# Optimization experiments

Measured on AMD Instinct MI355X. Metric: run time of the kernel, lower is better.

## Reference

```python
import jax, jax.numpy as jnp
import numpy as np

B, L, D = 2048, 64, 300   # batch, words per sentence, embedding dim (== kernel_size)
C = 512                    # conv out_channels
H, O = 2048, 1             # fc hidden, fc output


def setup_inputs() -> dict:
    key = jax.random.key(0)
    ks = jax.random.split(key, 8)
    s = 0.05
    return {
        "x1": jax.random.normal(ks[0], (B, L, D), jnp.float32),
        "x2": jax.random.normal(ks[1], (B, L, D), jnp.float32),
        # Conv1d(in=1, out=C, kernel=D) weight is [C,1,D]; stored as [C,D]
        "Wc": jax.random.normal(ks[2], (C, D), jnp.float32) * s,
        "bc": jax.random.normal(ks[3], (C,), jnp.float32) * s,
        "W1": jax.random.normal(ks[4], (H, 2 * C), jnp.float32) * s,
        "b1": jax.random.normal(ks[5], (H,), jnp.float32) * s,
        "W2": jax.random.normal(ks[6], (O, H), jnp.float32) * s,
        "b2": jax.random.normal(ks[7], (O,), jnp.float32) * s,
    }


def reference(x1, x2, Wc, bc, W1, b1, W2, b2):
    # Per-word Conv1d(kernel=D) + ReLU is a full-width filter == linear map D->C.
    # Batch all words in one einsum instead of the original Python loop.
    def encode(x):
        h = jax.nn.relu(jnp.einsum('bld,cd->blc', x, Wc) + bc)  # [B,L,C]
        return jnp.max(h, axis=1)                                # max over words -> [B,C]

    e1 = encode(x1)
    e2 = encode(x2)
    feat = jnp.concatenate([e1 - e2, e1 * e2], axis=1)           # [B,2C]
    h = jnp.tanh(feat @ W1.T + b1)                               # [B,H]
    return h @ W2.T + b2                                         # [B,O]
```

## Files before the change

kernel.cpp:

```cpp
#include <hip/hip_runtime.h>


#define B_SZ 2048
#define L_SZ 64
#define D_SZ 300
#define C_SZ 512
#define H_SZ 2048
#define KPAD 320
#define NKC 40
#define LDSPITCH 328

typedef __bf16 bf16x8 __attribute__((ext_vector_type(8)));
typedef float f32x4 __attribute__((ext_vector_type(4)));

__device__ __forceinline__ unsigned short f2bf(float f) {
  unsigned int u = __float_as_uint(f);
  u += 0x7fffu + ((u >> 16) & 1u);
  return (unsigned short)(u >> 16);
}

__global__ __launch_bounds__(256)
void convert_kernel(const float* __restrict__ Wc, const float* __restrict__ W1,
                    unsigned short* __restrict__ WcSwz, unsigned short* __restrict__ W1Swz) {
  int id = blockIdx.x * 256 + threadIdx.x;
  if (id < C_SZ * NKC) {
    int c = id / NKC, kc = id - c * NKC;
    unsigned short tmp[8];
    #pragma unroll
    for (int i = 0; i < 8; ++i) {
      int k = kc * 8 + i;
      tmp[i] = (k < D_SZ) ? f2bf(Wc[c * D_SZ + k]) : (unsigned short)0;
    }
    unsigned short* dst = WcSwz + (((c >> 4) * NKC + kc) * 16 + (c & 15)) * 8;
    *reinterpret_cast<uint4*>(dst) = *reinterpret_cast<uint4*>(tmp);
    return;
  }
  id -= C_SZ * NKC;
  if (id < H_SZ * 128) {
    int j = id >> 7, kc = id & 127;
    const float* src = W1 + (size_t)j * 1024 + kc * 8;
    unsigned short tmp[8];
    #pragma unroll
    for (int i = 0; i < 8; ++i) tmp[i] = f2bf(src[i]);
    unsigned short* dst = W1Swz + (((j >> 4) * 128 + kc) * 16 + (j & 15)) * 8;
    *reinterpret_cast<uint4*>(dst) = *reinterpret_cast<uint4*>(tmp);
  }
}

__global__ __launch_bounds__(256)
void encode_kernel(const float* __restrict__ x1, const float* __restrict__ x2,
                   const unsigned short* __restrict__ WcSwz,
                   const float* __restrict__ bc, float* __restrict__ e) {
  const int b = blockIdx.x, z = blockIdx.y;
  const float* __restrict__ x = (z ? x2 : x1) + (size_t)b * (L_SZ * D_SZ);
  __shared__ unsigned short xs[L_SZ * LDSPITCH];
  const int tid = threadIdx.x;

  const float4* __restrict__ xv = reinterpret_cast<const float4*>(x);
  for (int i = tid; i < (L_SZ * D_SZ / 4); i += 256) {
    float4 v = xv[i];
    int word = i / 75, col = (i - word * 75) * 4;
    unsigned int lo = (unsigned int)f2bf(v.x) | ((unsigned int)f2bf(v.y) << 16);
    unsigned int hi = (unsigned int)f2bf(v.z) | ((unsigned int)f2bf(v.w) << 16);
    *reinterpret_cast<uint2*>(&xs[word * LDSPITCH + col]) = make_uint2(lo, hi);
  }
  for (int i = tid; i < L_SZ * (KPAD - D_SZ); i += 256) {
    int word = i / 20, c = D_SZ + (i - word * 20);
    xs[word * LDSPITCH + c] = 0;
  }
  __syncthreads();

  const int wave = tid >> 6, lane = tid & 63;
  const int l16 = lane & 15, quad = lane >> 4;
  const int koff = quad * 8;

  f32x4 acc[4][8];
  #pragma unroll
  for (int mt = 0; mt < 4; ++mt)
    #pragma unroll
    for (int nt = 0; nt < 8; ++nt)
      #pragma unroll
      for (int r = 0; r < 4; ++r) acc[mt][nt][r] = 0.f;

  #pragma unroll
  for (int ks = 0; ks < KPAD / 32; ++ks) {
    bf16x8 a[4];
    #pragma unroll
    for (int mt = 0; mt < 4; ++mt)
      a[mt] = *reinterpret_cast<const bf16x8*>(&xs[(mt * 16 + l16) * LDSPITCH + ks * 32 + koff]);
    #pragma unroll
    for (int nt = 0; nt < 8; ++nt) {
      const unsigned short* bp =
          WcSwz + ((((wave * 8 + nt) * NKC) + ks * 4 + quad) * 16 + l16) * 8;
      bf16x8 bw = *reinterpret_cast<const bf16x8*>(bp);
      #pragma unroll
      for (int mt = 0; mt < 4; ++mt)
        acc[mt][nt] = __builtin_amdgcn_mfma_f32_16x16x32_bf16(a[mt], bw, acc[mt][nt], 0, 0, 0);
    }
  }

  #pragma unroll
  for (int nt = 0; nt < 8; ++nt) {
    int c = wave * 128 + nt * 16 + l16;
    float bias = bc[c];
    float v = 0.f;
    #pragma unroll
    for (int mt = 0; mt < 4; ++mt)
      #pragma unroll
      for (int r = 0; r < 4; ++r)
        v = fmaxf(v, acc[mt][nt][r] + bias);
    v = fmaxf(v, __shfl_xor(v, 16));
    v = fmaxf(v, __shfl_xor(v, 32));
    if (quad == 0)
      e[((size_t)z * B_SZ + b) * C_SZ + c] = v;
  }
}

__global__ __launch_bounds__(256)
void feat_kernel(const float* __restrict__ e, unsigned short* __restrict__ featSwz) {
  int id = blockIdx.x * 256 + threadIdx.x;
  if (id >= B_SZ * 128) return;
  int b = id >> 7, kc = id & 127;
  unsigned short tmp[8];
  #pragma unroll
  for (int i = 0; i < 8; ++i) {
    int k = kc * 8 + i, c = k & 511;
    float a = e[(size_t)b * C_SZ + c];
    float bb = e[(size_t)B_SZ * C_SZ + (size_t)b * C_SZ + c];
    tmp[i] = f2bf((k < C_SZ) ? (a - bb) : (a * bb));
  }
  unsigned short* dst = featSwz + (((b >> 4) * 128 + kc) * 16 + (b & 15)) * 8;
  *reinterpret_cast<uint4*>(dst) = *reinterpret_cast<uint4*>(tmp);
}

__global__ __launch_bounds__(256, 4)
void fc1_kernel(const unsigned short* __restrict__ featSwz,
                const unsigned short* __restrict__ W1Swz,
                const float* __restrict__ b1, const float* __restrict__ W2,
                float* __restrict__ partial) {
  const int mbase = blockIdx.x * 32;
  const int tid = threadIdx.x;
  const int wave = tid >> 6, lane = tid & 63;
  const int l16 = lane & 15, quad = lane >> 4;
  const int nbase = blockIdx.y * 128 + wave * 32;

  f32x4 acc[2][2];
  #pragma unroll
  for (int mt = 0; mt < 2; ++mt)
    #pragma unroll
    for (int nt = 0; nt < 2; ++nt)
      #pragma unroll
      for (int r = 0; r < 4; ++r) acc[mt][nt][r] = 0.f;

  #pragma unroll 4
  for (int ks = 0; ks < 32; ++ks) {
    bf16x8 a[2], bw[2];
    #pragma unroll
    for (int mt = 0; mt < 2; ++mt)
      a[mt] = *reinterpret_cast<const bf16x8*>(
          featSwz + (((size_t)(blockIdx.x * 2 + mt) * 128 + ks * 4 + quad) * 16 + l16) * 8);
    #pragma unroll
    for (int nt = 0; nt < 2; ++nt)
      bw[nt] = *reinterpret_cast<const bf16x8*>(
          W1Swz + (((size_t)(blockIdx.y * 8 + wave * 2 + nt) * 128 + ks * 4 + quad) * 16 + l16) * 8);
    #pragma unroll
    for (int mt = 0; mt < 2; ++mt)
      #pragma unroll
      for (int nt = 0; nt < 2; ++nt)
        acc[mt][nt] = __builtin_amdgcn_mfma_f32_16x16x32_bf16(a[mt], bw[nt], acc[mt][nt], 0, 0, 0);
  }

  float c[2][4];
  #pragma unroll
  for (int mt = 0; mt < 2; ++mt)
    #pragma unroll
    for (int r = 0; r < 4; ++r) c[mt][r] = 0.f;

  #pragma unroll
  for (int nt = 0; nt < 2; ++nt) {
    int j = nbase + nt * 16 + l16;
    float bias = b1[j];
    float w2 = W2[j];
    #pragma unroll
    for (int mt = 0; mt < 2; ++mt)
      #pragma unroll
      for (int r = 0; r < 4; ++r) {
        float pre = acc[mt][nt][r] + bias;
        pre = fminf(fmaxf(pre, -15.f), 15.f);
        float ex = __expf(2.f * pre);
        c[mt][r] += w2 * ((ex - 1.f) / (ex + 1.f));
      }
  }
  #pragma unroll
  for (int off = 1; off <= 8; off <<= 1)
    #pragma unroll
    for (int mt = 0; mt < 2; ++mt)
      #pragma unroll
      for (int r = 0; r < 4; ++r)
        c[mt][r] += __shfl_xor(c[mt][r], off);

  if (l16 == 0) {
    int slice = blockIdx.y * 4 + wave;
    #pragma unroll
    for (int mt = 0; mt < 2; ++mt)
      #pragma unroll
      for (int r = 0; r < 4; ++r) {
        int brow = mbase + mt * 16 + quad * 4 + r;
        partial[(size_t)slice * B_SZ + brow] = c[mt][r];
      }
  }
}

__global__ __launch_bounds__(256)
void finalize_kernel(const float* __restrict__ partial, const float* __restrict__ b2,
                     float* __restrict__ out) {
  int b = blockIdx.x * 256 + threadIdx.x;
  float s = b2[0];
  #pragma unroll 8
  for (int i = 0; i < 64; ++i) s += partial[(size_t)i * B_SZ + b];
  out[b] = s;
}

extern "C" void kernel_launch(void* const* d_in, const int* in_sizes, int n_in,
                              void* d_out, int out_size, void* d_ws, size_t ws_size,
                              hipStream_t stream) {
  const float* x1 = (const float*)d_in[0];
  const float* x2 = (const float*)d_in[1];
  const float* Wc = (const float*)d_in[2];
  const float* bc = (const float*)d_in[3];
  const float* W1 = (const float*)d_in[4];
  const float* b1 = (const float*)d_in[5];
  const float* W2 = (const float*)d_in[6];
  const float* b2 = (const float*)d_in[7];

  char* ws = (char*)d_ws;
  unsigned short* WcSwz   = (unsigned short*)(ws);
  unsigned short* W1Swz   = (unsigned short*)(ws + 327680);
  float*          e       = (float*)(ws + 4521984);
  unsigned short* featSwz = (unsigned short*)(ws + 12910592);
  float*          partial = (float*)(ws + 17104896);

  {
    int total = C_SZ * NKC + H_SZ * 128;
    convert_kernel<<<(total + 255) / 256, 256, 0, stream>>>(Wc, W1, WcSwz, W1Swz);
  }
  encode_kernel<<<dim3(B_SZ, 2), 256, 0, stream>>>(x1, x2, WcSwz, bc, e);
  feat_kernel<<<(B_SZ * 128 + 255) / 256, 256, 0, stream>>>(e, featSwz);
  fc1_kernel<<<dim3(B_SZ / 32, H_SZ / 128), 256, 0, stream>>>(featSwz, W1Swz, b1, W2, partial);
  finalize_kernel<<<B_SZ / 256, 256, 0, stream>>>(partial, b2, (float*)d_out);
}
```

Baseline: 489.3 us.

## K-major swizzled layouts, register double-buffering, and larger fc1 tiles

Reorders the swizzled bf16 layouts of Wc, W1 and feat so that the k-chunk index is outermost, giving contiguous loads per k-step. Both the encode and fc1 MFMA loops now prefetch the next k-step's operands into registers while the current step computes. fc1 tiles grow from 32x32 to 64x64 per wave-group, halving the number of partial slices that finalize has to reduce. Register pressure rises, so launch bounds are set to 2 blocks per CU, which lowers occupancy.

```diff
diff --git a/kernel.cpp b/kernel.cpp
--- a/kernel.cpp
+++ b/kernel.cpp
@@ -31,7 +31,7 @@
       int k = kc * 8 + i;
       tmp[i] = (k < D_SZ) ? f2bf(Wc[c * D_SZ + k]) : (unsigned short)0;
     }
-    unsigned short* dst = WcSwz + (((c >> 4) * NKC + kc) * 16 + (c & 15)) * 8;
+    unsigned short* dst = WcSwz + (((kc * 32 + (c >> 4)) * 16) + (c & 15)) * 8;
     *reinterpret_cast<uint4*>(dst) = *reinterpret_cast<uint4*>(tmp);
     return;
   }
@@ -42,12 +42,12 @@
     unsigned short tmp[8];
     #pragma unroll
     for (int i = 0; i < 8; ++i) tmp[i] = f2bf(src[i]);
-    unsigned short* dst = W1Swz + (((j >> 4) * 128 + kc) * 16 + (j & 15)) * 8;
+    unsigned short* dst = W1Swz + (((kc * 128 + (j >> 4)) * 16) + (j & 15)) * 8;
     *reinterpret_cast<uint4*>(dst) = *reinterpret_cast<uint4*>(tmp);
   }
 }
 
-__global__ __launch_bounds__(256)
+__global__ __launch_bounds__(256, 2)
 void encode_kernel(const float* __restrict__ x1, const float* __restrict__ x2,
                    const unsigned short* __restrict__ WcSwz,
                    const float* __restrict__ bc, float* __restrict__ e) {
@@ -72,7 +72,6 @@
 
   const int wave = tid >> 6, lane = tid & 63;
   const int l16 = lane & 15, quad = lane >> 4;
-  const int koff = quad * 8;
 
   f32x4 acc[4][8];
   #pragma unroll
@@ -82,20 +81,37 @@
       #pragma unroll
       for (int r = 0; r < 4; ++r) acc[mt][nt][r] = 0.f;
 
+  bf16x8 a[4], an[4], bw[8], bn[8];
+  #pragma unroll
+  for (int mt = 0; mt < 4; ++mt)
+    a[mt] = *reinterpret_cast<const bf16x8*>(&xs[(mt * 16 + l16) * LDSPITCH + quad * 8]);
+  #pragma unroll
+  for (int nt = 0; nt < 8; ++nt)
+    bw[nt] = *reinterpret_cast<const bf16x8*>(
+        WcSwz + (((quad * 32) + wave * 8 + nt) * 16 + l16) * 8);
+
   #pragma unroll
   for (int ks = 0; ks < KPAD / 32; ++ks) {
-    bf16x8 a[4];
-    #pragma unroll
-    for (int mt = 0; mt < 4; ++mt)
-      a[mt] = *reinterpret_cast<const bf16x8*>(&xs[(mt * 16 + l16) * LDSPITCH + ks * 32 + koff]);
-    #pragma unroll
-    for (int nt = 0; nt < 8; ++nt) {
-      const unsigned short* bp =
-          WcSwz + ((((wave * 8 + nt) * NKC) + ks * 4 + quad) * 16 + l16) * 8;
-      bf16x8 bw = *reinterpret_cast<const bf16x8*>(bp);
+    if (ks < KPAD / 32 - 1) {
       #pragma unroll
       for (int mt = 0; mt < 4; ++mt)
-        acc[mt][nt] = __builtin_amdgcn_mfma_f32_16x16x32_bf16(a[mt], bw, acc[mt][nt], 0, 0, 0);
+        an[mt] = *reinterpret_cast<const bf16x8*>(
+            &xs[(mt * 16 + l16) * LDSPITCH + (ks + 1) * 32 + quad * 8]);
+      #pragma unroll
+      for (int nt = 0; nt < 8; ++nt)
+        bn[nt] = *reinterpret_cast<const bf16x8*>(
+            WcSwz + ((((ks + 1) * 4 + quad) * 32 + wave * 8 + nt) * 16 + l16) * 8);
+    }
+    #pragma unroll
+    for (int nt = 0; nt < 8; ++nt)
+      #pragma unroll
+      for (int mt = 0; mt < 4; ++mt)
+        acc[mt][nt] = __builtin_amdgcn_mfma_f32_16x16x32_bf16(a[mt], bw[nt], acc[mt][nt], 0, 0, 0);
+    if (ks < KPAD / 32 - 1) {
+      #pragma unroll
+      for (int mt = 0; mt < 4; ++mt) a[mt] = an[mt];
+      #pragma unroll
+      for (int nt = 0; nt < 8; ++nt) bw[nt] = bn[nt];
     }
   }
 
@@ -129,60 +145,77 @@
     float bb = e[(size_t)B_SZ * C_SZ + (size_t)b * C_SZ + c];
     tmp[i] = f2bf((k < C_SZ) ? (a - bb) : (a * bb));
   }
-  unsigned short* dst = featSwz + (((b >> 4) * 128 + kc) * 16 + (b & 15)) * 8;
+  unsigned short* dst = featSwz + (((kc * 128 + (b >> 4)) * 16) + (b & 15)) * 8;
   *reinterpret_cast<uint4*>(dst) = *reinterpret_cast<uint4*>(tmp);
 }
 
-__global__ __launch_bounds__(256, 4)
+__global__ __launch_bounds__(256, 2)
 void fc1_kernel(const unsigned short* __restrict__ featSwz,
                 const unsigned short* __restrict__ W1Swz,
                 const float* __restrict__ b1, const float* __restrict__ W2,
                 float* __restrict__ partial) {
-  const int mbase = blockIdx.x * 32;
   const int tid = threadIdx.x;
   const int wave = tid >> 6, lane = tid & 63;
   const int l16 = lane & 15, quad = lane >> 4;
-  const int nbase = blockIdx.y * 128 + wave * 32;
-
-  f32x4 acc[2][2];
-  #pragma unroll
-  for (int mt = 0; mt < 2; ++mt)
-    #pragma unroll
-    for (int nt = 0; nt < 2; ++nt)
+  const int mtile = blockIdx.x * 4;
+  const int ntile = blockIdx.y * 16 + wave * 4;
+
+  f32x4 acc[4][4];
+  #pragma unroll
+  for (int mt = 0; mt < 4; ++mt)
+    #pragma unroll
+    for (int nt = 0; nt < 4; ++nt)
       #pragma unroll
       for (int r = 0; r < 4; ++r) acc[mt][nt][r] = 0.f;
 
-  #pragma unroll 4
+  bf16x8 a[4], an[4], bw[4], bn[4];
+  #pragma unroll
+  for (int mt = 0; mt < 4; ++mt)
+    a[mt] = *reinterpret_cast<const bf16x8*>(
+        featSwz + (((size_t)quad * 128 + mtile + mt) * 16 + l16) * 8);
+  #pragma unroll
+  for (int nt = 0; nt < 4; ++nt)
+    bw[nt] = *reinterpret_cast<const bf16x8*>(
+        W1Swz + (((size_t)quad * 128 + ntile + nt) * 16 + l16) * 8);
+
+  #pragma unroll
   for (int ks = 0; ks < 32; ++ks) {
-    bf16x8 a[2], bw[2];
-    #pragma unroll
-    for (int mt = 0; mt < 2; ++mt)
-      a[mt] = *reinterpret_cast<const bf16x8*>(
-          featSwz + (((size_t)(blockIdx.x * 2 + mt) * 128 + ks * 4 + quad) * 16 + l16) * 8);
-    #pragma unroll
-    for (int nt = 0; nt < 2; ++nt)
-      bw[nt] = *reinterpret_cast<const bf16x8*>(
-          W1Swz + (((size_t)(blockIdx.y * 8 + wave * 2 + nt) * 128 + ks * 4 + quad) * 16 + l16) * 8);
-    #pragma unroll
-    for (int mt = 0; mt < 2; ++mt)
-      #pragma unroll
-      for (int nt = 0; nt < 2; ++nt)
+    if (ks < 31) {
+      #pragma unroll
+      for (int mt = 0; mt < 4; ++mt)
+        an[mt] = *reinterpret_cast<const bf16x8*>(
+            featSwz + ((((size_t)(ks + 1) * 4 + quad) * 128 + mtile + mt) * 16 + l16) * 8);
+      #pragma unroll
+      for (int nt = 0; nt < 4; ++nt)
+        bn[nt] = *reinterpret_cast<const bf16x8*>(
+            W1Swz + ((((size_t)(ks + 1) * 4 + quad) * 128 + ntile + nt) * 16 + l16) * 8);
+    }
+    #pragma unroll
+    for (int mt = 0; mt < 4; ++mt)
+      #pragma unroll
+      for (int nt = 0; nt < 4; ++nt)
         acc[mt][nt] = __builtin_amdgcn_mfma_f32_16x16x32_bf16(a[mt], bw[nt], acc[mt][nt], 0, 0, 0);
-  }
-
-  float c[2][4];
-  #pragma unroll
-  for (int mt = 0; mt < 2; ++mt)
+    if (ks < 31) {
+      #pragma unroll
+      for (int mt = 0; mt < 4; ++mt) a[mt] = an[mt];
+      #pragma unroll
+      for (int nt = 0; nt < 4; ++nt) bw[nt] = bn[nt];
+    }
+  }
+
+  float c[4][4];
+  #pragma unroll
+  for (int mt = 0; mt < 4; ++mt)
     #pragma unroll
     for (int r = 0; r < 4; ++r) c[mt][r] = 0.f;
 
   #pragma unroll
-  for (int nt = 0; nt < 2; ++nt) {
-    int j = nbase + nt * 16 + l16;
+  for (int nt = 0; nt < 4; ++nt) {
+    int j = blockIdx.y * 256 + wave * 64 + nt * 16 + l16;
     float bias = b1[j];
     float w2 = W2[j];
     #pragma unroll
-    for (int mt = 0; mt < 2; ++mt)
+    for (int mt = 0; mt < 4; ++mt)
       #pragma unroll
       for (int r = 0; r < 4; ++r) {
         float pre = acc[mt][nt][r] + bias;
@@ -194,7 +227,7 @@
   #pragma unroll
   for (int off = 1; off <= 8; off <<= 1)
     #pragma unroll
-    for (int mt = 0; mt < 2; ++mt)
+    for (int mt = 0; mt < 4; ++mt)
       #pragma unroll
       for (int r = 0; r < 4; ++r)
         c[mt][r] += __shfl_xor(c[mt][r], off);
@@ -202,10 +235,10 @@
   if (l16 == 0) {
     int slice = blockIdx.y * 4 + wave;
     #pragma unroll
-    for (int mt = 0; mt < 2; ++mt)
+    for (int mt = 0; mt < 4; ++mt)
       #pragma unroll
       for (int r = 0; r < 4; ++r) {
-        int brow = mbase + mt * 16 + quad * 4 + r;
+        int brow = blockIdx.x * 64 + mt * 16 + quad * 4 + r;
         partial[(size_t)slice * B_SZ + brow] = c[mt][r];
       }
   }
@@ -217,7 +250,7 @@
   int b = blockIdx.x * 256 + threadIdx.x;
   float s = b2[0];
   #pragma unroll 8
-  for (int i = 0; i < 64; ++i) s += partial[(size_t)i * B_SZ + b];
+  for (int i = 0; i < 32; ++i) s += partial[(size_t)i * B_SZ + b];
   out[b] = s;
 }
 
@@ -246,6 +279,6 @@
   }
   encode_kernel<<<dim3(B_SZ, 2), 256, 0, stream>>>(x1, x2, WcSwz, bc, e);
   feat_kernel<<<(B_SZ * 128 + 255) / 256, 256, 0, stream>>>(e, featSwz);
-  fc1_kernel<<<dim3(B_SZ / 32, H_SZ / 128), 256, 0, stream>>>(featSwz, W1Swz, b1, W2, partial);
+  fc1_kernel<<<dim3(H_SZ / 64, H_SZ / 256), 256, 0, stream>>>(featSwz, W1Swz, b1, W2, partial);
   finalize_kernel<<<B_SZ / 256, 256, 0, stream>>>(partial, b2, (float*)d_out);
 }
```

Result: slower. 576.4 us (+17.8%).

## Make swizzled weight layouts k-major and split encode channels across two blocks

Applied to the files above, without the earlier changes.

The swizzled bf16 layouts for Wc, W1 and the fc1 features now put the k-chunk outermost instead of the row tile. At each k step, neighbouring tiles then sit next to each other in memory. The encode kernel is split into two blocks per sentence, each covering half the conv channels with fewer accumulators, and gets a 3-blocks-per-CU launch bound to raise occupancy. The cost is that each sentence's input is loaded and converted to bf16 twice, once per half. The fc1 grid uses H_SZ/32, which equals B_SZ/32 here, so it is unchanged in effect.

```diff
diff --git a/kernel.cpp b/kernel.cpp
--- a/kernel.cpp
+++ b/kernel.cpp
@@ -31,7 +31,7 @@
       int k = kc * 8 + i;
       tmp[i] = (k < D_SZ) ? f2bf(Wc[c * D_SZ + k]) : (unsigned short)0;
     }
-    unsigned short* dst = WcSwz + (((c >> 4) * NKC + kc) * 16 + (c & 15)) * 8;
+    unsigned short* dst = WcSwz + (((kc * 32 + (c >> 4)) * 16) + (c & 15)) * 8;
     *reinterpret_cast<uint4*>(dst) = *reinterpret_cast<uint4*>(tmp);
     return;
   }
@@ -42,16 +42,16 @@
     unsigned short tmp[8];
     #pragma unroll
     for (int i = 0; i < 8; ++i) tmp[i] = f2bf(src[i]);
-    unsigned short* dst = W1Swz + (((j >> 4) * 128 + kc) * 16 + (j & 15)) * 8;
+    unsigned short* dst = W1Swz + (((kc * 128 + (j >> 4)) * 16) + (j & 15)) * 8;
     *reinterpret_cast<uint4*>(dst) = *reinterpret_cast<uint4*>(tmp);
   }
 }
 
-__global__ __launch_bounds__(256)
+__global__ __launch_bounds__(256, 3)
 void encode_kernel(const float* __restrict__ x1, const float* __restrict__ x2,
                    const unsigned short* __restrict__ WcSwz,
                    const float* __restrict__ bc, float* __restrict__ e) {
-  const int b = blockIdx.x, z = blockIdx.y;
+  const int h = blockIdx.x, b = blockIdx.y, z = blockIdx.z;
   const float* __restrict__ x = (z ? x2 : x1) + (size_t)b * (L_SZ * D_SZ);
   __shared__ unsigned short xs[L_SZ * LDSPITCH];
   const int tid = threadIdx.x;
@@ -72,13 +72,12 @@
 
   const int wave = tid >> 6, lane = tid & 63;
   const int l16 = lane & 15, quad = lane >> 4;
-  const int koff = quad * 8;
-
-  f32x4 acc[4][8];
+
+  f32x4 acc[4][4];
   #pragma unroll
   for (int mt = 0; mt < 4; ++mt)
     #pragma unroll
-    for (int nt = 0; nt < 8; ++nt)
+    for (int nt = 0; nt < 4; ++nt)
       #pragma unroll
       for (int r = 0; r < 4; ++r) acc[mt][nt][r] = 0.f;
 
@@ -87,12 +86,12 @@
     bf16x8 a[4];
     #pragma unroll
     for (int mt = 0; mt < 4; ++mt)
-      a[mt] = *reinterpret_cast<const bf16x8*>(&xs[(mt * 16 + l16) * LDSPITCH + ks * 32 + koff]);
-    #pragma unroll
-    for (int nt = 0; nt < 8; ++nt) {
-      const unsigned short* bp =
-          WcSwz + ((((wave * 8 + nt) * NKC) + ks * 4 + quad) * 16 + l16) * 8;
-      bf16x8 bw = *reinterpret_cast<const bf16x8*>(bp);
+      a[mt] = *reinterpret_cast<const bf16x8*>(&xs[(mt * 16 + l16) * LDSPITCH + ks * 32 + quad * 8]);
+    #pragma unroll
+    for (int nt = 0; nt < 4; ++nt) {
+      int ctile = h * 16 + wave * 4 + nt;
+      bf16x8 bw = *reinterpret_cast<const bf16x8*>(
+          WcSwz + (((ks * 4 + quad) * 32 + ctile) * 16 + l16) * 8);
       #pragma unroll
       for (int mt = 0; mt < 4; ++mt)
         acc[mt][nt] = __builtin_amdgcn_mfma_f32_16x16x32_bf16(a[mt], bw, acc[mt][nt], 0, 0, 0);
@@ -100,8 +99,8 @@
   }
 
   #pragma unroll
-  for (int nt = 0; nt < 8; ++nt) {
-    int c = wave * 128 + nt * 16 + l16;
+  for (int nt = 0; nt < 4; ++nt) {
+    int c = (h * 16 + wave * 4 + nt) * 16 + l16;
     float bias = bc[c];
     float v = 0.f;
     #pragma unroll
@@ -129,7 +128,7 @@
     float bb = e[(size_t)B_SZ * C_SZ + (size_t)b * C_SZ + c];
     tmp[i] = f2bf((k < C_SZ) ? (a - bb) : (a * bb));
   }
-  unsigned short* dst = featSwz + (((b >> 4) * 128 + kc) * 16 + (b & 15)) * 8;
+  unsigned short* dst = featSwz + (((kc * 128 + (b >> 4)) * 16) + (b & 15)) * 8;
   *reinterpret_cast<uint4*>(dst) = *reinterpret_cast<uint4*>(tmp);
 }
 
@@ -138,11 +137,11 @@
                 const unsigned short* __restrict__ W1Swz,
                 const float* __restrict__ b1, const float* __restrict__ W2,
                 float* __restrict__ partial) {
-  const int mbase = blockIdx.x * 32;
   const int tid = threadIdx.x;
   const int wave = tid >> 6, lane = tid & 63;
   const int l16 = lane & 15, quad = lane >> 4;
-  const int nbase = blockIdx.y * 128 + wave * 32;
+  const int mt0 = blockIdx.x * 2;
+  const int nt0 = blockIdx.y * 8 + wave * 2;
 
   f32x4 acc[2][2];
   #pragma unroll
@@ -158,11 +157,11 @@
     #pragma unroll
     for (int mt = 0; mt < 2; ++mt)
       a[mt] = *reinterpret_cast<const bf16x8*>(
-          featSwz + (((size_t)(blockIdx.x * 2 + mt) * 128 + ks * 4 + quad) * 16 + l16) * 8);
+          featSwz + ((((size_t)ks * 4 + quad) * 128 + mt0 + mt) * 16 + l16) * 8);
     #pragma unroll
     for (int nt = 0; nt < 2; ++nt)
       bw[nt] = *reinterpret_cast<const bf16x8*>(
-          W1Swz + (((size_t)(blockIdx.y * 8 + wave * 2 + nt) * 128 + ks * 4 + quad) * 16 + l16) * 8);
+          W1Swz + ((((size_t)ks * 4 + quad) * 128 + nt0 + nt) * 16 + l16) * 8);
     #pragma unroll
     for (int mt = 0; mt < 2; ++mt)
       #pragma unroll
@@ -178,7 +177,7 @@
 
   #pragma unroll
   for (int nt = 0; nt < 2; ++nt) {
-    int j = nbase + nt * 16 + l16;
+    int j = (nt0 + nt) * 16 + l16;
     float bias = b1[j];
     float w2 = W2[j];
     #pragma unroll
@@ -205,7 +204,7 @@
     for (int mt = 0; mt < 2; ++mt)
       #pragma unroll
       for (int r = 0; r < 4; ++r) {
-        int brow = mbase + mt * 16 + quad * 4 + r;
+        int brow = (mt0 + mt) * 16 + quad * 4 + r;
         partial[(size_t)slice * B_SZ + brow] = c[mt][r];
       }
   }
@@ -244,8 +243,8 @@
     int total = C_SZ * NKC + H_SZ * 128;
     convert_kernel<<<(total + 255) / 256, 256, 0, stream>>>(Wc, W1, WcSwz, W1Swz);
   }
-  encode_kernel<<<dim3(B_SZ, 2), 256, 0, stream>>>(x1, x2, WcSwz, bc, e);
+  encode_kernel<<<dim3(2, B_SZ, 2), 256, 0, stream>>>(x1, x2, WcSwz, bc, e);
   feat_kernel<<<(B_SZ * 128 + 255) / 256, 256, 0, stream>>>(e, featSwz);
-  fc1_kernel<<<dim3(B_SZ / 32, H_SZ / 128), 256, 0, stream>>>(featSwz, W1Swz, b1, W2, partial);
+  fc1_kernel<<<dim3(H_SZ / 32, H_SZ / 128), 256, 0, stream>>>(featSwz, W1Swz, b1, W2, partial);
   finalize_kernel<<<B_SZ / 256, 256, 0, stream>>>(partial, b2, (float*)d_out);
 }
```

Result: slower. 515.2 us (+5.3%).
